# Optimization experiments

Measured on AMD Instinct MI355X. Metric: run time of the kernel, lower is better.

Reference implementation:

```python
import jax, jax.numpy as jnp
import numpy as np

N, D, P, T, M, H = 8192, 64, 32, 1, 50, 512
INTERVAL = 1.0
SIGMA = 1.0


def setup_inputs() -> dict:
    key = jax.random.key(0)
    k = jax.random.split(key, 9)
    in_dim = 1 + D + P  # [s, X, Y_t]
    return {
        "X0": jax.random.normal(k[0], (N, D), jnp.float32),
        "V0": jax.random.normal(k[1], (N,), jnp.float32),
        "Y": jax.random.normal(k[2], (N, T, P), jnp.float32),
        "theta": jax.random.normal(k[3], (D,), jnp.float32),
        "W1": jax.random.normal(k[4], (in_dim, H), jnp.float32) / np.sqrt(in_dim),
        "b1": jnp.zeros((H,), jnp.float32),
        "W2": jax.random.normal(k[5], (H, D), jnp.float32) / np.sqrt(H),
        "b2": jnp.zeros((D,), jnp.float32),
        "noise": jax.random.normal(k[6], (M, N, D), jnp.float32),
        "obs_index": 0,
    }


def reference(X0, V0, Y, theta, W1, b1, W2, b2, noise, obs_index):
    dt = jnp.float32(INTERVAL / M)
    sqrt_dt = jnp.sqrt(dt)
    Yt = Y[:, obs_index, :]  # (N, p) observation at this index

    def z_net(s, X):
        # Z_net(t, s, X, Y): MLP over [s, X, Y_t] -> (N, d)
        s_col = jnp.full((X.shape[0], 1), s, X.dtype)
        h = jnp.tanh(jnp.concatenate([s_col, X, Yt], axis=1) @ W1 + b1)
        return h @ W2 + b2

    def step(carry, xs):
        X, V = carry
        s, w = xs
        Wm = sqrt_dt * w  # Brownian increment
        Z = z_net(s, X)
        control = -jax.lax.stop_gradient(Z)  # -Z.detach()
        drift_V = 0.5 * jnp.sum(Z * Z, axis=1) + jnp.sum(control * Z, axis=1)
        V_new = V + dt * drift_V + jnp.sum(Z * Wm, axis=1)
        drift_X = (theta - X) + SIGMA * control  # b(theta, X) = theta - X (OU)
        X_new = X + dt * drift_X + SIGMA * Wm
        return (X_new, V_new), None

    times = jnp.arange(M, dtype=X0.dtype) * dt
    (X, V), _ = jax.lax.scan(step, (X0, V0), (times, noise))
    return X, V
```

## Files before the change

kernel.cpp:

```cpp
#include <hip/hip_runtime.h>
#include <hip/hip_bf16.h>

typedef __attribute__((ext_vector_type(4))) float f32x4;
typedef __attribute__((ext_vector_type(8))) short bf16x8;

#define NPART 8192
#define DDIM 64
#define PDIM 32
#define MSTEPS 50
#define HDIM 512
#define A_LD 72
#define H_LD 520

__device__ __forceinline__ short f2bf(float f) {
  unsigned u = __builtin_bit_cast(unsigned, f);
  u = (u + 0x7fffu + ((u >> 16) & 1u)) >> 16;
  return (short)u;
}

__device__ __forceinline__ float fast_tanh(float xv) {
  float t = __expf(2.0f * xv);
  return 1.0f - 2.0f * __builtin_amdgcn_rcpf(t + 1.0f);
}

__device__ __forceinline__ unsigned pack_pair(float own) {
  int oi = __builtin_amdgcn_mov_dpp(__builtin_bit_cast(int, own),
                                    0xB1 , 0xF, 0xF, true);
  float other = __builtin_bit_cast(float, oi);
  unsigned out;
  asm("v_cvt_pk_bf16_f32 %0, %1, %2" : "=v"(out) : "v"(own), "v"(other));
  return out;
}

__global__ __launch_bounds__(1024) void sde_kernel(
    const float* __restrict__ X0, const float* __restrict__ V0,
    const float* __restrict__ Y, const float* __restrict__ theta,
    const float* __restrict__ W1, const float* __restrict__ b1,
    const float* __restrict__ W2, const float* __restrict__ b2,
    const float* __restrict__ noise, const int* __restrict__ obs_index,
    float* __restrict__ out) {
  __shared__ __align__(16) short lds_h[32 * H_LD];
  __shared__ __align__(16) short lds_a[32 * A_LD];
  __shared__ __align__(16) float lds_p[8 * 64 * 4];

  const int tid = threadIdx.x;
  const int w = tid >> 6;
  const int lane = tid & 63;
  const int c = lane & 15;
  const int g = lane >> 4;
  const int pb = blockIdx.x * 32;
  const int kh = w & 1, ntw = (w >> 1) & 3, mtw = w >> 3;

  const float dt = 0.02f;
  const float sqdt = sqrtf(dt);

  {
    int m = tid >> 5, p = tid & 31;
    lds_p[m * PDIM + p] =
        Y[(size_t)(pb + m) * PDIM + (size_t)obs_index[0] * PDIM + p];
  }

  float x[4] = {0.f, 0.f, 0.f, 0.f};
  if (kh == 0) {
    #pragma unroll
    for (int r = 0; r < 4; ++r) {
      int m = 16 * mtw + 4 * g + r;
      x[r] = X0[(size_t)(pb + m) * DDIM + 16 * ntw + c];
      lds_a[m * A_LD + 16 * ntw + c] = f2bf(x[r]);
    }
  }
  __syncthreads();

  const int nj0 = 32 * w + c;
  float cy[2][2][4];
  float rv0[2] = {W1[nj0], W1[nj0 + 16]};
  {
    float bv0 = b1[nj0], bv1 = b1[nj0 + 16];
    #pragma unroll
    for (int mt = 0; mt < 2; ++mt)
      #pragma unroll
      for (int r = 0; r < 4; ++r) { cy[mt][0][r] = bv0; cy[mt][1][r] = bv1; }
    for (int p = 0; p < PDIM; ++p) {
      float wv0 = W1[(size_t)(65 + p) * HDIM + nj0];
      float wv1 = W1[(size_t)(65 + p) * HDIM + nj0 + 16];
      #pragma unroll
      for (int mt = 0; mt < 2; ++mt)
        #pragma unroll
        for (int r = 0; r < 4; ++r) {
          float yv = lds_p[(16 * mt + 4 * g + r) * PDIM + p];
          cy[mt][0][r] = fmaf(yv, wv0, cy[mt][0][r]);
          cy[mt][1][r] = fmaf(yv, wv1, cy[mt][1][r]);
        }
    }
  }

  bf16x8 bfr[2][2];
  #pragma unroll
  for (int e = 0; e < 2; ++e)
    #pragma unroll
    for (int kt = 0; kt < 2; ++kt)
      #pragma unroll
      for (int i = 0; i < 8; ++i)
        bfr[e][kt][i] =
            f2bf(W1[(size_t)(1 + 32 * kt + 8 * g + i) * HDIM + nj0 + 16 * e]);

  bf16x8 w2f[8];
  #pragma unroll
  for (int kt = 0; kt < 8; ++kt)
    #pragma unroll
    for (int i = 0; i < 8; ++i)
      w2f[kt][i] =
          f2bf(W2[(size_t)(256 * kh + 32 * kt + 8 * g + i) * DDIM + 16 * ntw + c]);

  const float thv = theta[16 * ntw + c];
  const float b2v = b2[16 * ntw + c];
  float vacc[4] = {0.f, 0.f, 0.f, 0.f};

  __syncthreads();

  for (int st = 0; st < MSTEPS; ++st) {
    const float s = st * dt;

    float wm[4];
    if (kh == 0) {
      const float* np_ =
          noise + ((size_t)st * NPART + pb + 16 * mtw + 4 * g) * DDIM + 16 * ntw + c;
      #pragma unroll
      for (int r = 0; r < 4; ++r) wm[r] = np_[(size_t)r * DDIM];
    }

    #pragma unroll
    for (int mt = 0; mt < 2; ++mt) {
      const int abase = (16 * mt + c) * A_LD + 8 * g;
      bf16x8 af0 = *reinterpret_cast<const bf16x8*>(&lds_a[abase]);
      bf16x8 af1 = *reinterpret_cast<const bf16x8*>(&lds_a[abase + 32]);
      #pragma unroll
      for (int e = 0; e < 2; ++e) {
        f32x4 acc = {0.f, 0.f, 0.f, 0.f};
        acc = __builtin_amdgcn_mfma_f32_16x16x32_bf16(af0, bfr[e][0], acc, 0, 0, 0);
        acc = __builtin_amdgcn_mfma_f32_16x16x32_bf16(af1, bfr[e][1], acc, 0, 0, 0);
        float sb = s * rv0[e];
        unsigned pk[4];
        #pragma unroll
        for (int r = 0; r < 4; ++r)
          pk[r] = pack_pair(fast_tanh(acc[r] + cy[mt][e][r] + sb));
        if (!(lane & 1)) {
          #pragma unroll
          for (int r = 0; r < 4; ++r)
            *reinterpret_cast<unsigned*>(
                &lds_h[(16 * mt + 4 * g + r) * H_LD + nj0 + 16 * e]) = pk[r];
        }
      }
    }

    __syncthreads();

    f32x4 acc2 = {0.f, 0.f, 0.f, 0.f};
    {
      const int hbase = (16 * mtw + c) * H_LD + 256 * kh + 8 * g;
      #pragma unroll
      for (int kt = 0; kt < 8; ++kt)
        acc2 = __builtin_amdgcn_mfma_f32_16x16x32_bf16(
            *reinterpret_cast<const bf16x8*>(&lds_h[hbase + 32 * kt]), w2f[kt],
            acc2, 0, 0, 0);
    }
    float* pslot = &lds_p[((mtw * 4 + ntw) * 64 + lane) * 4];
    if (kh) *reinterpret_cast<f32x4*>(pslot) = acc2;

    __syncthreads();

    if (!kh) {
      f32x4 part = *reinterpret_cast<const f32x4*>(pslot);
      unsigned apk[4];
      #pragma unroll
      for (int r = 0; r < 4; ++r) {
        float z = acc2[r] + part[r] + b2v;
        float wmr = sqdt * wm[r];
        vacc[r] = fmaf(z, wmr - 0.5f * dt * z, vacc[r]);
        x[r] = x[r] + dt * (thv - x[r] - z) + wmr;
        apk[r] = pack_pair(x[r]);
      }
      if (!(lane & 1)) {
        #pragma unroll
        for (int r = 0; r < 4; ++r)
          *reinterpret_cast<unsigned*>(
              &lds_a[(16 * mtw + 4 * g + r) * A_LD + 16 * ntw + c]) = apk[r];
      }
    }

    __syncthreads();
  }

  if (!kh) {
    #pragma unroll
    for (int r = 0; r < 4; ++r)
      out[(size_t)(pb + 16 * mtw + 4 * g + r) * DDIM + 16 * ntw + c] = x[r];
    #pragma unroll
    for (int mask = 1; mask <= 8; mask <<= 1)
      #pragma unroll
      for (int r = 0; r < 4; ++r) vacc[r] += __shfl_xor(vacc[r], mask);
    if (c == 0) {
      #pragma unroll
      for (int r = 0; r < 4; ++r)
        lds_p[(16 * mtw + 4 * g + r) * 4 + ntw] = vacc[r];
    }
  }
  __syncthreads();
  if (tid < 32)
    out[(size_t)NPART * DDIM + pb + tid] =
        V0[pb + tid] + lds_p[tid * 4] + lds_p[tid * 4 + 1] +
        lds_p[tid * 4 + 2] + lds_p[tid * 4 + 3];
}

extern "C" void kernel_launch(void* const* d_in, const int* in_sizes, int n_in,
                              void* d_out, int out_size, void* d_ws, size_t ws_size,
                              hipStream_t stream) {
  sde_kernel<<<256, 1024, 0, stream>>>(
      (const float*)d_in[0], (const float*)d_in[1], (const float*)d_in[2],
      (const float*)d_in[3], (const float*)d_in[4], (const float*)d_in[5],
      (const float*)d_in[6], (const float*)d_in[7], (const float*)d_in[8],
      (const int*)d_in[9], (float*)d_out);
}
```

Measured before the change: 272.5 us.

## Halve particles per block to 16 and launch 512 blocks of 512 threads

```diff
diff --git a/kernel.cpp b/kernel.cpp
--- a/kernel.cpp
+++ b/kernel.cpp
@@ -9,6 +9,7 @@
 #define PDIM 32
 #define MSTEPS 50
 #define HDIM 512
+#define MB 16
 #define A_LD 72
 #define H_LD 520
 
@@ -32,77 +33,74 @@
   return out;
 }
 
-__global__ __launch_bounds__(1024) void sde_kernel(
+__global__ __launch_bounds__(512, 4) void sde_kernel(
     const float* __restrict__ X0, const float* __restrict__ V0,
     const float* __restrict__ Y, const float* __restrict__ theta,
     const float* __restrict__ W1, const float* __restrict__ b1,
     const float* __restrict__ W2, const float* __restrict__ b2,
     const float* __restrict__ noise, const int* __restrict__ obs_index,
     float* __restrict__ out) {
-  __shared__ __align__(16) short lds_h[32 * H_LD];
-  __shared__ __align__(16) short lds_a[32 * A_LD];
-  __shared__ __align__(16) float lds_p[8 * 64 * 4];
+  __shared__ __align__(16) short lds_h[MB * H_LD];
+  __shared__ __align__(16) short lds_a[MB * A_LD];
+  __shared__ __align__(16) float lds_p[4 * 64 * 4];
 
   const int tid = threadIdx.x;
   const int w = tid >> 6;
   const int lane = tid & 63;
   const int c = lane & 15;
   const int g = lane >> 4;
-  const int pb = blockIdx.x * 32;
-  const int kh = w & 1, ntw = (w >> 1) & 3, mtw = w >> 3;
+  const int pb = blockIdx.x * MB;
+  const int ntw = w & 3, kh = w >> 2;
 
   const float dt = 0.02f;
   const float sqdt = sqrtf(dt);
 
   {
     int m = tid >> 5, p = tid & 31;
-    lds_p[m * PDIM + p] =
-        Y[(size_t)(pb + m) * PDIM + (size_t)obs_index[0] * PDIM + p];
+    lds_p[tid] = Y[(size_t)(pb + m) * PDIM + (size_t)obs_index[0] * PDIM + p];
   }
 
   float x[4] = {0.f, 0.f, 0.f, 0.f};
   if (kh == 0) {
     #pragma unroll
     for (int r = 0; r < 4; ++r) {
-      int m = 16 * mtw + 4 * g + r;
+      int m = 4 * g + r;
       x[r] = X0[(size_t)(pb + m) * DDIM + 16 * ntw + c];
       lds_a[m * A_LD + 16 * ntw + c] = f2bf(x[r]);
     }
   }
   __syncthreads();
 
-  const int nj0 = 32 * w + c;
-  float cy[2][2][4];
-  float rv0[2] = {W1[nj0], W1[nj0 + 16]};
-  {
-    float bv0 = b1[nj0], bv1 = b1[nj0 + 16];
-    #pragma unroll
-    for (int mt = 0; mt < 2; ++mt)
-      #pragma unroll
-      for (int r = 0; r < 4; ++r) { cy[mt][0][r] = bv0; cy[mt][1][r] = bv1; }
-    for (int p = 0; p < PDIM; ++p) {
-      float wv0 = W1[(size_t)(65 + p) * HDIM + nj0];
-      float wv1 = W1[(size_t)(65 + p) * HDIM + nj0 + 16];
-      #pragma unroll
-      for (int mt = 0; mt < 2; ++mt)
-        #pragma unroll
-        for (int r = 0; r < 4; ++r) {
-          float yv = lds_p[(16 * mt + 4 * g + r) * PDIM + p];
-          cy[mt][0][r] = fmaf(yv, wv0, cy[mt][0][r]);
-          cy[mt][1][r] = fmaf(yv, wv1, cy[mt][1][r]);
-        }
-    }
-  }
-
-  bf16x8 bfr[2][2];
+  const int nj0 = 64 * w + c;
+  f32x4 cy[4];
+  float rv0[4];
   #pragma unroll
-  for (int e = 0; e < 2; ++e)
+  for (int j = 0; j < 4; ++j) {
+    rv0[j] = W1[nj0 + 16 * j];
+    float bv = b1[nj0 + 16 * j];
+    cy[j] = (f32x4){bv, bv, bv, bv};
+  }
+  for (int p = 0; p < PDIM; ++p) {
+    float yv[4];
+    #pragma unroll
+    for (int r = 0; r < 4; ++r) yv[r] = lds_p[(4 * g + r) * PDIM + p];
+    #pragma unroll
+    for (int j = 0; j < 4; ++j) {
+      float wv = W1[(size_t)(65 + p) * HDIM + nj0 + 16 * j];
+      #pragma unroll
+      for (int r = 0; r < 4; ++r) cy[j][r] = fmaf(yv[r], wv, cy[j][r]);
+    }
+  }
+
+  bf16x8 bfr[4][2];
+  #pragma unroll
+  for (int j = 0; j < 4; ++j)
     #pragma unroll
     for (int kt = 0; kt < 2; ++kt)
       #pragma unroll
       for (int i = 0; i < 8; ++i)
-        bfr[e][kt][i] =
-            f2bf(W1[(size_t)(1 + 32 * kt + 8 * g + i) * HDIM + nj0 + 16 * e]);
+        bfr[j][kt][i] =
+            f2bf(W1[(size_t)(1 + 32 * kt + 8 * g + i) * HDIM + nj0 + 16 * j]);
 
   bf16x8 w2f[8];
   #pragma unroll
@@ -124,47 +122,45 @@
     float wm[4];
     if (kh == 0) {
       const float* np_ =
-          noise + ((size_t)st * NPART + pb + 16 * mtw + 4 * g) * DDIM + 16 * ntw + c;
+          noise + ((size_t)st * NPART + pb + 4 * g) * DDIM + 16 * ntw + c;
       #pragma unroll
       for (int r = 0; r < 4; ++r) wm[r] = np_[(size_t)r * DDIM];
     }
 
-    #pragma unroll
-    for (int mt = 0; mt < 2; ++mt) {
-      const int abase = (16 * mt + c) * A_LD + 8 * g;
+    {
+      const int abase = c * A_LD + 8 * g;
       bf16x8 af0 = *reinterpret_cast<const bf16x8*>(&lds_a[abase]);
       bf16x8 af1 = *reinterpret_cast<const bf16x8*>(&lds_a[abase + 32]);
       #pragma unroll
-      for (int e = 0; e < 2; ++e) {
-        f32x4 acc = {0.f, 0.f, 0.f, 0.f};
-        acc = __builtin_amdgcn_mfma_f32_16x16x32_bf16(af0, bfr[e][0], acc, 0, 0, 0);
-        acc = __builtin_amdgcn_mfma_f32_16x16x32_bf16(af1, bfr[e][1], acc, 0, 0, 0);
-        float sb = s * rv0[e];
+      for (int j = 0; j < 4; ++j) {
+        f32x4 acc = cy[j];
+        acc = __builtin_amdgcn_mfma_f32_16x16x32_bf16(af0, bfr[j][0], acc, 0, 0, 0);
+        acc = __builtin_amdgcn_mfma_f32_16x16x32_bf16(af1, bfr[j][1], acc, 0, 0, 0);
         unsigned pk[4];
         #pragma unroll
         for (int r = 0; r < 4; ++r)
-          pk[r] = pack_pair(fast_tanh(acc[r] + cy[mt][e][r] + sb));
+          pk[r] = pack_pair(fast_tanh(fmaf(s, rv0[j], acc[r])));
         if (!(lane & 1)) {
           #pragma unroll
           for (int r = 0; r < 4; ++r)
             *reinterpret_cast<unsigned*>(
-                &lds_h[(16 * mt + 4 * g + r) * H_LD + nj0 + 16 * e]) = pk[r];
+                &lds_h[(4 * g + r) * H_LD + nj0 + 16 * j]) = pk[r];
         }
       }
     }
 
     __syncthreads();
 
-    f32x4 acc2 = {0.f, 0.f, 0.f, 0.f};
+    f32x4 acc2 = kh ? (f32x4){0.f, 0.f, 0.f, 0.f} : (f32x4){b2v, b2v, b2v, b2v};
     {
-      const int hbase = (16 * mtw + c) * H_LD + 256 * kh + 8 * g;
+      const int hbase = c * H_LD + 256 * kh + 8 * g;
       #pragma unroll
       for (int kt = 0; kt < 8; ++kt)
         acc2 = __builtin_amdgcn_mfma_f32_16x16x32_bf16(
             *reinterpret_cast<const bf16x8*>(&lds_h[hbase + 32 * kt]), w2f[kt],
             acc2, 0, 0, 0);
     }
-    float* pslot = &lds_p[((mtw * 4 + ntw) * 64 + lane) * 4];
+    float* pslot = &lds_p[(ntw * 64 + lane) * 4];
     if (kh) *reinterpret_cast<f32x4*>(pslot) = acc2;
 
     __syncthreads();
@@ -174,17 +170,17 @@
       unsigned apk[4];
       #pragma unroll
       for (int r = 0; r < 4; ++r) {
-        float z = acc2[r] + part[r] + b2v;
+        float z = acc2[r] + part[r];
         float wmr = sqdt * wm[r];
-        vacc[r] = fmaf(z, wmr - 0.5f * dt * z, vacc[r]);
-        x[r] = x[r] + dt * (thv - x[r] - z) + wmr;
+        vacc[r] = fmaf(z, fmaf(-0.5f * dt, z, wmr), vacc[r]);
+        x[r] = fmaf(dt, thv - x[r] - z, x[r]) + wmr;
         apk[r] = pack_pair(x[r]);
       }
       if (!(lane & 1)) {
         #pragma unroll
         for (int r = 0; r < 4; ++r)
           *reinterpret_cast<unsigned*>(
-              &lds_a[(16 * mtw + 4 * g + r) * A_LD + 16 * ntw + c]) = apk[r];
+              &lds_a[(4 * g + r) * A_LD + 16 * ntw + c]) = apk[r];
       }
     }
 
@@ -194,7 +190,7 @@
   if (!kh) {
     #pragma unroll
     for (int r = 0; r < 4; ++r)
-      out[(size_t)(pb + 16 * mtw + 4 * g + r) * DDIM + 16 * ntw + c] = x[r];
+      out[(size_t)(pb + 4 * g + r) * DDIM + 16 * ntw + c] = x[r];
     #pragma unroll
     for (int mask = 1; mask <= 8; mask <<= 1)
       #pragma unroll
@@ -202,11 +198,11 @@
     if (c == 0) {
       #pragma unroll
       for (int r = 0; r < 4; ++r)
-        lds_p[(16 * mtw + 4 * g + r) * 4 + ntw] = vacc[r];
+        lds_p[(4 * g + r) * 4 + ntw] = vacc[r];
     }
   }
   __syncthreads();
-  if (tid < 32)
+  if (tid < MB)
     out[(size_t)NPART * DDIM + pb + tid] =
         V0[pb + tid] + lds_p[tid * 4] + lds_p[tid * 4 + 1] +
         lds_p[tid * 4 + 2] + lds_p[tid * 4 + 3];
@@ -215,7 +211,7 @@
 extern "C" void kernel_launch(void* const* d_in, const int* in_sizes, int n_in,
                               void* d_out, int out_size, void* d_ws, size_t ws_size,
                               hipStream_t stream) {
-  sde_kernel<<<256, 1024, 0, stream>>>(
+  sde_kernel<<<512, 512, 0, stream>>>(
       (const float*)d_in[0], (const float*)d_in[1], (const float*)d_in[2],
       (const float*)d_in[3], (const float*)d_in[4], (const float*)d_in[5],
       (const float*)d_in[6], (const float*)d_in[7], (const float*)d_in[8],
```

Result: slower. 283.2 us (+4.0%).
